# Kernel optimization log

Measured on AMD Instinct MI355X. Metric: run time of the kernel, lower is better.

Reference implementation:

```python
import jax, jax.numpy as jnp
import numpy as np

N = 65536      # num ref nodes
M = 65536      # num query nodes
E = 1572864    # num edges (avg degree 24)
K0 = 27        # num kernels (3x3x3 neighborhood)
D1 = 64        # input channels
D2 = 64        # output channels


def setup_inputs() -> dict:
    key = jax.random.key(0)
    k1, k2, k3, k4, k5, k6 = jax.random.split(key, 6)
    # kernel init mirrors initialize_kernel_weight (uniform in [-bound, bound])
    fan_in = D1 * K0
    gain = float(np.sqrt(2.0 / (1.0 + 5.0)))  # leaky_relu gain with slope sqrt(5)
    std = gain / np.sqrt(fan_in)
    bound = float(np.sqrt(3.0) * std)
    kernel = jax.random.uniform(k1, (K0, D1, D2), minval=-bound, maxval=bound, dtype=jnp.float32)
    ref_feat = jax.random.normal(k2, (N, D1), dtype=jnp.float32)
    e_kernel = jax.random.randint(k3, (E,), 0, K0)
    e_ref = jax.random.randint(k4, (E,), 0, N)
    e_query = jax.random.randint(k5, (E,), 0, M)
    e_weight = jax.random.uniform(k6, (E,), dtype=jnp.float32)
    return {
        "kernel": kernel,
        "ref_feat": ref_feat,
        "e_kernel": e_kernel,
        "e_ref": e_ref,
        "e_query": e_query,
        "num_queries": M,
        "e_weight": e_weight,
    }


def reference(kernel, ref_feat, e_kernel, e_ref, e_query, num_queries, e_weight):
    # Math of MessagePassing.forward:
    #   query_feat[m] = sum_{edges e: e_query[e]==m} w_e * (ref_feat[e_ref[e]] @ kernel[e_kernel[e]])
    # Efficient form: precompute each node's transform under every kernel
    # (N*K0*D1*D2 dense GEMM), then gather per edge and scatter-reduce.
    transformed = jnp.einsum('nd,kdo->nko', ref_feat, kernel)   # [N, K0, D2]
    msgs = transformed[e_ref, e_kernel] * e_weight[:, None]      # [E, D2]
    query_feat = jax.ops.segment_sum(msgs, e_query, num_segments=num_queries)  # [M, D2]
    return query_feat
```

## Files before the change

kernel.cpp:

```cpp
#include <hip/hip_runtime.h>

#define DIN 64
#define DOUT 64
#define MAXK 32
#define KSPLIT 8
#define KS4 5
#define QG 128

typedef __bf16 bf16x8 __attribute__((ext_vector_type(8)));
typedef float  f32x4  __attribute__((ext_vector_type(4)));
typedef unsigned int u32x4 __attribute__((ext_vector_type(4)));

static __device__ inline unsigned short f2b(float x) {
    return __builtin_bit_cast(unsigned short, (__bf16)x);
}
static __device__ inline float b2f(unsigned short u) {
    return __uint_as_float(((unsigned int)u) << 16);
}

__global__ __launch_bounds__(256) void pre_kernel(
    const float* __restrict__ W, unsigned short* __restrict__ Wt, int total,
    const int* __restrict__ eq, int E, int* __restrict__ qcount, int HB)
{
    const int t = threadIdx.x;
    if ((int)blockIdx.x < HB) {
        __shared__ int l[512];
        l[t] = 0; l[t + 256] = 0;
        __syncthreads();
        const int stride = HB * 256;
        for (int i = (int)blockIdx.x * 256 + t; i < E; i += stride)
            atomicAdd(&l[((unsigned)eq[i]) >> 7], 1);
        __syncthreads();
        int v0 = l[t];       if (v0) atomicAdd(&qcount[t], v0);
        int v1 = l[t + 256]; if (v1) atomicAdd(&qcount[t + 256], v1);
    } else {
        int i = ((int)blockIdx.x - HB) * 256 + t;
        if (i < total) {
            int j    = i & 7;
            int lane = (i >> 3) & 63;
            int h    = (i >> 9) & 1;
            int tt   = (i >> 10) & 3;
            int k    = i >> 12;
            int col  = lane & 15;
            int quad = lane >> 4;
            int d1 = h * 32 + quad * 8 + j;
            int d2 = tt * 16 + col;
            Wt[i] = f2b(W[(k * 64 + d1) * 64 + d2]);
        }
    }
}

__global__ void p1_scan_kernel(const int* __restrict__ qcount,
                               int* __restrict__ gbase, int* __restrict__ gcursor,
                               int* __restrict__ qstart, int NB, int M, int E) {
    __shared__ int sh[1024];
    int t = threadIdx.x;
    int v = (t < NB) ? qcount[t] : 0;
    sh[t] = v;
    __syncthreads();
    #pragma unroll
    for (int o = 1; o < 1024; o <<= 1) {
        int x = (t >= o) ? sh[t - o] : 0;
        __syncthreads();
        sh[t] += x;
        __syncthreads();
    }
    int ex = sh[t] - v;
    if (t < NB) { gbase[t] = ex; gcursor[t] = ex; }
    if (t == 0) qstart[M] = E;
}


static __device__ __forceinline__ void phaseA_body16(
    const float* __restrict__ ref,
    const unsigned short* __restrict__ Wt,
    unsigned short* __restrict__ T,
    int K0, int Nn, int nblk, int k0, int k1, char* lds)
{
    const int t    = threadIdx.x;
    const int lane = t & 63;
    const int wid  = t >> 6;
    const int col  = lane & 15;
    const int quad = lane >> 4;
    const int n0   = nblk * 256 + wid * 16;
    const int row  = n0 + col;
    char* buf = lds + wid * 2304;

    const float* rp = ref + (size_t)row * 64;
    f32x4 r0 = *reinterpret_cast<const f32x4*>(rp + quad * 8);
    f32x4 r1 = *reinterpret_cast<const f32x4*>(rp + quad * 8 + 4);
    f32x4 r2 = *reinterpret_cast<const f32x4*>(rp + 32 + quad * 8);
    f32x4 r3 = *reinterpret_cast<const f32x4*>(rp + 32 + quad * 8 + 4);
    bf16x8 b0, b1;
    #pragma unroll
    for (int i = 0; i < 4; ++i) {
        b0[i]     = (__bf16)r0[i];
        b0[4 + i] = (__bf16)r1[i];
        b1[i]     = (__bf16)r2[i];
        b1[4 + i] = (__bf16)r3[i];
    }

    const int rrow = lane >> 2;
    const int rq   = lane & 3;

    for (int k = k0; k < k1; ++k) {
        const unsigned short* Wk = Wt + (size_t)k * 4096;
        #pragma unroll
        for (int tt = 0; tt < 4; ++tt) {
            const unsigned short* ap = Wk + (size_t)tt * 1024 + lane * 8;
            bf16x8 a0 = *reinterpret_cast<const bf16x8*>(ap);
            bf16x8 a1 = *reinterpret_cast<const bf16x8*>(ap + 512);
            f32x4 c = {0.f, 0.f, 0.f, 0.f};
            c = __builtin_amdgcn_mfma_f32_16x16x32_bf16(a0, b0, c, 0, 0, 0);
            c = __builtin_amdgcn_mfma_f32_16x16x32_bf16(a1, b1, c, 0, 0, 0);
            unsigned int lo = (unsigned int)f2b(c[0]) | ((unsigned int)f2b(c[1]) << 16);
            unsigned int hi = (unsigned int)f2b(c[2]) | ((unsigned int)f2b(c[3]) << 16);
            *reinterpret_cast<uint2*>(buf + col * 144 + tt * 32 + quad * 8) =
                make_uint2(lo, hi);
        }
        u32x4 v0 = *reinterpret_cast<const u32x4*>(buf + rrow * 144 + rq * 32);
        u32x4 v1 = *reinterpret_cast<const u32x4*>(buf + rrow * 144 + rq * 32 + 16);
        size_t gb = ((size_t)k * Nn + n0 + rrow) * 64 + rq * 16;
        *reinterpret_cast<u32x4*>(T + gb)     = v0;
        *reinterpret_cast<u32x4*>(T + gb + 8) = v1;
    }
}


__global__ __launch_bounds__(1024) void fusedA_scatter_kernel(
    const float* __restrict__ ref, const unsigned short* __restrict__ Wt,
    unsigned short* __restrict__ T, int K0, int Nn, int SCB, int NA2,
    const int* __restrict__ eq, const int* __restrict__ er,
    const int* __restrict__ ek, const float* __restrict__ ew,
    int E, int* __restrict__ gcursor, uint2* __restrict__ tmp)
{
    __shared__ __align__(16) char ldsbuf[16 * 2304];
    __shared__ int bin[512];
    __shared__ int base[512];
    const int t = threadIdx.x;

    if ((int)blockIdx.x < SCB) {
        if (t < 512) bin[t] = 0;
        __syncthreads();
        const int i0 = (int)blockIdx.x * 8192;
        unsigned key[8];
        unsigned rank[8];
        uint2 pay[8];
        #pragma unroll
        for (int u = 0; u < 8; ++u) {
            int i = i0 + u * 1024 + t;
            if (i < E) {
                int q = eq[i];
                unsigned b = ((unsigned)q) >> 7;
                key[u] = b;
                rank[u] = atomicAdd(&bin[b], 1);
                pay[u] = make_uint2((unsigned)er[i] | ((unsigned)ek[i] << 16) |
                                    ((unsigned)(q & (QG - 1)) << 21),
                                    __float_as_uint(ew[i]));
            } else {
                key[u] = 0xFFFFFFFFu;
            }
        }
        __syncthreads();
        if (t < 512) {
            int c = bin[t];
            if (c) base[t] = atomicAdd(&gcursor[t], c);
        }
        __syncthreads();
        #pragma unroll
        for (int u = 0; u < 8; ++u) {
            if (key[u] != 0xFFFFFFFFu)
                tmp[(size_t)base[key[u]] + rank[u]] = pay[u];
        }
    } else {
        const int ab   = (int)blockIdx.x - SCB;
        const int nblk = ab % NA2;
        const int ky   = ab / NA2;
        const int kch  = (K0 + KSPLIT - 1) / KSPLIT;
        const int k0   = ky * kch;
        if (k0 >= K0) return;
        int k1 = k0 + kch;
        if (k1 > K0) k1 = K0;
        phaseA_body16(ref, Wt, T, K0, Nn, nblk, k0, k1, ldsbuf);
    }
}

__global__ __launch_bounds__(1024) void fusedA_p2_kernel(
    const float* __restrict__ ref, const unsigned short* __restrict__ Wt,
    unsigned short* __restrict__ T, int K0, int Nn, int NB, int NA2,
    const uint2* __restrict__ tmp, const int* __restrict__ gbase,
    const int* __restrict__ qcount, uint2* __restrict__ rec,
    int* __restrict__ qstart)
{
    __shared__ __align__(16) char ldsbuf[16 * 2304];
    __shared__ int fine[QG];
    __shared__ int foff[QG];
    __shared__ int vsave[QG];
    const int t = threadIdx.x;

    if ((int)blockIdx.x < NB) {
        const int b = (int)blockIdx.x;
        const int s = gbase[b];
        const int L = qcount[b];
        if (t < QG) fine[t] = 0;
        __syncthreads();
        for (int i = t; i < L; i += 1024)
            atomicAdd(&fine[(tmp[s + i].x >> 21) & (QG - 1)], 1);
        __syncthreads();
        if (t < QG) vsave[t] = fine[t];
        __syncthreads();
        #pragma unroll
        for (int o = 1; o < QG; o <<= 1) {
            int x = (t >= o && t < QG) ? fine[t - o] : 0;
            __syncthreads();
            if (t < QG) fine[t] += x;
            __syncthreads();
        }
        if (t < QG) {
            int ex = fine[t] - vsave[t];
            foff[t] = ex;
            qstart[b * QG + t] = s + ex;
            fine[t] = 0;
        }
        __syncthreads();
        for (int i = t; i < L; i += 1024) {
            uint2 p = tmp[s + i];
            unsigned fb = (p.x >> 21) & (QG - 1);
            int r = atomicAdd(&fine[fb], 1);
            rec[(size_t)s + foff[fb] + r] = p;
        }
    } else {
        const int ab   = (int)blockIdx.x - NB;
        const int nblk = ab % NA2;
        const int ky   = KS4 + ab / NA2;
        const int kch  = (K0 + KSPLIT - 1) / KSPLIT;
        const int k0   = ky * kch;
        if (k0 >= K0) return;
        int k1 = k0 + kch;
        if (k1 > K0) k1 = K0;
        phaseA_body16(ref, Wt, T, K0, Nn, nblk, k0, k1, ldsbuf);
    }
}


__global__ __launch_bounds__(256) void phaseB_kernel(
    const unsigned short* __restrict__ T,
    const uint2* __restrict__ rec,
    const int* __restrict__ qstart,
    float* __restrict__ out, int Nn)
{
    const int lane = threadIdx.x & 63;
    const int wid  = threadIdx.x >> 6;
    const int q    = blockIdx.x * 4 + wid;

    int beg = qstart[q];
    int end = qstart[q + 1];
    int cnt = end - beg;
    float acc = 0.f;

    if (cnt <= 64) {
        uint2 rv = make_uint2(0u, 0u);
        if (lane < cnt) rv = rec[beg + lane];
        int j = 0;
        for (; j + 8 <= cnt; j += 8) {
            float partial[8];
            #pragma unroll
            for (int u = 0; u < 8; ++u) {
                unsigned mx = (unsigned)__builtin_amdgcn_readlane((int)rv.x, j + u);
                unsigned mw = (unsigned)__builtin_amdgcn_readlane((int)rv.y, j + u);
                unsigned off = (((mx >> 16) & 31) * (unsigned)Nn + (mx & 0xFFFFu)) * 64u
                               + (unsigned)lane;
                partial[u] = __uint_as_float(mw) * b2f(T[off]);
            }
            #pragma unroll
            for (int u = 0; u < 8; ++u) acc += partial[u];
        }
        for (; j < cnt; ++j) {
            unsigned mx = (unsigned)__builtin_amdgcn_readlane((int)rv.x, j);
            unsigned mw = (unsigned)__builtin_amdgcn_readlane((int)rv.y, j);
            unsigned off = (((mx >> 16) & 31) * (unsigned)Nn + (mx & 0xFFFFu)) * 64u
                           + (unsigned)lane;
            acc = fmaf(__uint_as_float(mw), b2f(T[off]), acc);
        }
    } else {
        for (int j = beg; j < end; ++j) {
            uint2 v0 = rec[j];
            unsigned m0 = __builtin_amdgcn_readfirstlane(v0.x);
            float w0 = __uint_as_float(__builtin_amdgcn_readfirstlane(v0.y));
            unsigned off = (((m0 >> 16) & 31) * (unsigned)Nn + (m0 & 0xFFFFu)) * 64u
                           + (unsigned)lane;
            acc = fmaf(w0, b2f(T[off]), acc);
        }
    }
    out[(size_t)q * 64 + lane] = acc;
}


__global__ void hist_kernel(const int* __restrict__ ek, int E, int* __restrict__ counts) {
    __shared__ int l[MAXK];
    if (threadIdx.x < MAXK) l[threadIdx.x] = 0;
    __syncthreads();
    int stride = gridDim.x * blockDim.x;
    for (int i = blockIdx.x * blockDim.x + threadIdx.x; i < E; i += stride)
        atomicAdd(&l[ek[i]], 1);
    __syncthreads();
    if (threadIdx.x < MAXK) {
        int v = l[threadIdx.x];
        if (v) atomicAdd(&counts[threadIdx.x], v);
    }
}

__global__ void scan_kernel(const int* __restrict__ counts, int K,
                            int* __restrict__ start, int* __restrict__ cursor) {
    if (threadIdx.x == 0 && blockIdx.x == 0) {
        int acc = 0;
        for (int k = 0; k < K; ++k) {
            start[k] = acc;
            cursor[k] = acc;
            acc += counts[k];
        }
    }
}

__global__ void scatter_kernel(const int* __restrict__ ek, int E,
                               int* __restrict__ cursor, int* __restrict__ sorted) {
    __shared__ int lcnt[MAXK], lbase[MAXK], lpos[MAXK];
    if (threadIdx.x < MAXK) { lcnt[threadIdx.x] = 0; lpos[threadIdx.x] = 0; }
    __syncthreads();
    int i = blockIdx.x * blockDim.x + threadIdx.x;
    int k = 0;
    bool valid = (i < E);
    if (valid) { k = ek[i]; atomicAdd(&lcnt[k], 1); }
    __syncthreads();
    if (threadIdx.x < MAXK) {
        int v = lcnt[threadIdx.x];
        if (v) lbase[threadIdx.x] = atomicAdd(&cursor[threadIdx.x], v);
    }
    __syncthreads();
    if (valid) {
        int slot = lbase[k] + atomicAdd(&lpos[k], 1);
        sorted[slot] = i;
    }
}

__global__ __launch_bounds__(256) void mp_bucket_kernel(
    const float* __restrict__ W, const float* __restrict__ ref,
    const int* __restrict__ e_ref, const int* __restrict__ e_query,
    const float* __restrict__ e_weight, const int* __restrict__ sorted,
    const int* __restrict__ start, const int* __restrict__ counts,
    float* __restrict__ out)
{
    const int k = blockIdx.y;
    const int lane = threadIdx.x & 63;
    const int wid = threadIdx.x >> 6;

    float wreg[DIN];
    const float* Wk = W + k * DIN * DOUT;
    #pragma unroll
    for (int d = 0; d < DIN; ++d) wreg[d] = Wk[d * DOUT + lane];

    const int s = start[k];
    const int c = counts[k];
    const int nwaves = gridDim.x * 4;

    for (int i = blockIdx.x * 4 + wid; i < c; i += nwaves) {
        int eid = __builtin_amdgcn_readfirstlane(sorted[s + i]);
        int r = e_ref[eid];
        int q = e_query[eid];
        float w = e_weight[eid];
        const float* row = ref + r * DIN;
        float a0 = 0.f, a1 = 0.f, a2 = 0.f, a3 = 0.f;
        #pragma unroll
        for (int d = 0; d < DIN; d += 4) {
            a0 += row[d + 0] * wreg[d + 0];
            a1 += row[d + 1] * wreg[d + 1];
            a2 += row[d + 2] * wreg[d + 2];
            a3 += row[d + 3] * wreg[d + 3];
        }
        atomicAdd(&out[q * DOUT + lane], ((a0 + a1) + (a2 + a3)) * w);
    }
}


extern "C" void kernel_launch(void* const* d_in, const int* in_sizes, int n_in,
                              void* d_out, int out_size, void* d_ws, size_t ws_size,
                              hipStream_t stream) {
    const float* W        = (const float*)d_in[0];
    const float* ref      = (const float*)d_in[1];
    const int*   e_kernel = (const int*)d_in[2];
    const int*   e_ref    = (const int*)d_in[3];
    const int*   e_query  = (const int*)d_in[4];
    const float* e_weight = (const float*)d_in[6];

    const int K0 = in_sizes[0] / (DIN * DOUT);
    const int N  = in_sizes[1] / DIN;
    const int E  = in_sizes[2];
    const int M  = out_size / DOUT;
    const int KD = K0 * 64;
    const int NB = M / QG;

    float* out = (float*)d_out;

    size_t off = 0;
    auto alloc = [&](size_t bytes, size_t align) {
        off = (off + align - 1) / align * align;
        size_t r = off; off += bytes; return r;
    };
    size_t o_tmp     = alloc((size_t)E * 8, 16);
    size_t o_rec     = alloc((size_t)E * 8, 16);
    size_t o_qstart  = alloc((size_t)(M + 1) * 4, 4);
    size_t o_qcount  = alloc(1024 * 4, 4);
    size_t o_gbase   = alloc(1024 * 4, 4);
    size_t o_gcursor = alloc(1024 * 4, 4);
    size_t o_wt      = alloc((size_t)K0 * 4096 * 2, 16);
    size_t o_T       = alloc((size_t)N * KD * 2, 16);
    size_t needA = off;

    bool planA_ok = (ws_size >= needA) && (M % QG == 0) && (NB >= 1) && (NB <= 512) &&
                    (N % 256 == 0) && (N <= 65536) && (K0 <= 32);

    if (planA_ok) {
        char* ws = (char*)d_ws;
        uint2* tmp           = (uint2*)(ws + o_tmp);
        uint2* rec           = (uint2*)(ws + o_rec);
        int*  qstart         = (int*)(ws + o_qstart);
        int*  qcount         = (int*)(ws + o_qcount);
        int*  gbase          = (int*)(ws + o_gbase);
        int*  gcursor        = (int*)(ws + o_gcursor);
        unsigned short* Wt   = (unsigned short*)(ws + o_wt);
        unsigned short* T    = (unsigned short*)(ws + o_T);

        const int HB   = 512;
        const int CWB  = (K0 * 4096 + 255) / 256;
        const int SCB  = (E + 8191) / 8192;
        const int NA2  = N / 256;

        hipMemsetAsync(qcount, 0, 1024 * sizeof(int), stream);

        pre_kernel<<<HB + CWB, 256, 0, stream>>>(W, Wt, K0 * 4096,
                                                 e_query, E, qcount, HB);

        p1_scan_kernel<<<1, 1024, 0, stream>>>(qcount, gbase, gcursor, qstart, NB, M, E);

        fusedA_scatter_kernel<<<SCB + NA2 * KS4, 1024, 0, stream>>>(
            ref, Wt, T, K0, N, SCB, NA2,
            e_query, e_ref, e_kernel, e_weight, E, gcursor, tmp);

        fusedA_p2_kernel<<<NB + NA2 * (KSPLIT - KS4), 1024, 0, stream>>>(
            ref, Wt, T, K0, N, NB, NA2,
            tmp, gbase, qcount, rec, qstart);

        phaseB_kernel<<<M / 4, 256, 0, stream>>>(T, rec, qstart, out, N);
    } else {
        hipMemsetAsync(out, 0, (size_t)out_size * sizeof(float), stream);
        size_t needB = (size_t)(96 + E) * sizeof(int);
        if (ws_size >= needB) {
            int* ws_i   = (int*)d_ws;
            int* counts = ws_i;
            int* start  = ws_i + 32;
            int* cursor = ws_i + 64;
            int* sorted = ws_i + 96;
            hipMemsetAsync(counts, 0, 96 * sizeof(int), stream);
            hist_kernel<<<512, 256, 0, stream>>>(e_kernel, E, counts);
            scan_kernel<<<1, 64, 0, stream>>>(counts, K0, start, cursor);
            scatter_kernel<<<(E + 255) / 256, 256, 0, stream>>>(e_kernel, E, cursor, sorted);
            dim3 grid(64, K0);
            mp_bucket_kernel<<<grid, 256, 0, stream>>>(W, ref, e_ref, e_query, e_weight,
                                                       sorted, start, counts, out);
        }
    }
}
```

Before: 274.9 us.

## Fold scan into scatter kernel and skip unused transformed rows via usage map

Removes the separate single-block scan launch: each scatter block redoes the 512-entry prefix scan of the bucket counts itself and adds it to a zero-based cursor. The scatter pass also marks which (kernel, ref node) pairs are touched by any edge in a byte map, and the second-phase GEMM blocks skip the T stores for untouched rows. The k-range split between the two fused kernels changes from 8 slices to fixed 4-kernel chunks with the first 12 kernels in the first launch. This adds a memset of the map and a redundant scan per scatter block. With random edges about 41% of rows are untouched, so only part of the T writes in the second kernel are saved.

```diff
diff --git a/kernel.cpp b/kernel.cpp
--- a/kernel.cpp
+++ b/kernel.cpp
@@ -3,9 +3,8 @@
 #define DIN 64
 #define DOUT 64
 #define MAXK 32
-#define KSPLIT 8
-#define KS4 5
 #define QG 128
+#define KCH 4
 
 typedef __bf16 bf16x8 __attribute__((ext_vector_type(8)));
 typedef float  f32x4  __attribute__((ext_vector_type(4)));
@@ -17,6 +16,7 @@
 static __device__ inline float b2f(unsigned short u) {
     return __uint_as_float(((unsigned int)u) << 16);
 }
+
 
 __global__ __launch_bounds__(256) void pre_kernel(
     const float* __restrict__ W, unsigned short* __restrict__ Wt, int total,
@@ -50,32 +50,14 @@
     }
 }
 
-__global__ void p1_scan_kernel(const int* __restrict__ qcount,
-                               int* __restrict__ gbase, int* __restrict__ gcursor,
-                               int* __restrict__ qstart, int NB, int M, int E) {
-    __shared__ int sh[1024];
-    int t = threadIdx.x;
-    int v = (t < NB) ? qcount[t] : 0;
-    sh[t] = v;
-    __syncthreads();
-    #pragma unroll
-    for (int o = 1; o < 1024; o <<= 1) {
-        int x = (t >= o) ? sh[t - o] : 0;
-        __syncthreads();
-        sh[t] += x;
-        __syncthreads();
-    }
-    int ex = sh[t] - v;
-    if (t < NB) { gbase[t] = ex; gcursor[t] = ex; }
-    if (t == 0) qstart[M] = E;
-}
-
-
+
+template <bool MAPPED>
 static __device__ __forceinline__ void phaseA_body16(
     const float* __restrict__ ref,
     const unsigned short* __restrict__ Wt,
+    const unsigned char* __restrict__ map,
     unsigned short* __restrict__ T,
-    int K0, int Nn, int nblk, int k0, int k1, char* lds)
+    int Nn, int nblk, int k0, int k1, char* lds)
 {
     const int t    = threadIdx.x;
     const int lane = t & 63;
@@ -104,6 +86,8 @@
     const int rq   = lane & 3;
 
     for (int k = k0; k < k1; ++k) {
+        unsigned char use = 1;
+        if (MAPPED) use = map[(size_t)k * Nn + n0 + rrow];
         const unsigned short* Wk = Wt + (size_t)k * 4096;
         #pragma unroll
         for (int tt = 0; tt < 4; ++tt) {
@@ -120,28 +104,47 @@
         }
         u32x4 v0 = *reinterpret_cast<const u32x4*>(buf + rrow * 144 + rq * 32);
         u32x4 v1 = *reinterpret_cast<const u32x4*>(buf + rrow * 144 + rq * 32 + 16);
-        size_t gb = ((size_t)k * Nn + n0 + rrow) * 64 + rq * 16;
-        *reinterpret_cast<u32x4*>(T + gb)     = v0;
-        *reinterpret_cast<u32x4*>(T + gb + 8) = v1;
-    }
-}
-
-
-__global__ __launch_bounds__(1024) void fusedA_scatter_kernel(
+        if (use) {
+            size_t gb = ((size_t)k * Nn + n0 + rrow) * 64 + rq * 16;
+            *reinterpret_cast<u32x4*>(T + gb)     = v0;
+            *reinterpret_cast<u32x4*>(T + gb + 8) = v1;
+        }
+    }
+}
+
+
+__global__ __launch_bounds__(1024) void fused_scat_kernel(
     const float* __restrict__ ref, const unsigned short* __restrict__ Wt,
-    unsigned short* __restrict__ T, int K0, int Nn, int SCB, int NA2,
+    unsigned short* __restrict__ T, int K0, int Nn, int SCB, int NA2, int K1,
     const int* __restrict__ eq, const int* __restrict__ er,
     const int* __restrict__ ek, const float* __restrict__ ew,
-    int E, int* __restrict__ gcursor, uint2* __restrict__ tmp)
+    int E, const int* __restrict__ qcount, int* __restrict__ gbase,
+    int* __restrict__ gcursor, int* __restrict__ qstart, int M,
+    uint2* __restrict__ tmp, unsigned char* __restrict__ map)
 {
     __shared__ __align__(16) char ldsbuf[16 * 2304];
+    __shared__ int sh[512];
     __shared__ int bin[512];
     __shared__ int base[512];
     const int t = threadIdx.x;
 
     if ((int)blockIdx.x < SCB) {
+        int v = 0;
+        if (t < 512) { v = qcount[t]; sh[t] = v; }
+        __syncthreads();
+        #pragma unroll
+        for (int o = 1; o < 512; o <<= 1) {
+            int x = (t >= o && t < 512) ? sh[t - o] : 0;
+            __syncthreads();
+            if (t < 512) sh[t] += x;
+            __syncthreads();
+        }
+        if (t < 512) sh[t] -= v;
+        if ((int)blockIdx.x == 0 && t < 512) gbase[t] = sh[t];
+        if ((int)blockIdx.x == 0 && t == 0) qstart[M] = E;
         if (t < 512) bin[t] = 0;
         __syncthreads();
+
         const int i0 = (int)blockIdx.x * 8192;
         unsigned key[8];
         unsigned rank[8];
@@ -150,13 +153,16 @@
         for (int u = 0; u < 8; ++u) {
             int i = i0 + u * 1024 + t;
             if (i < E) {
-                int q = eq[i];
+                int q  = eq[i];
+                int rr = er[i];
+                int kk = ek[i];
                 unsigned b = ((unsigned)q) >> 7;
                 key[u] = b;
                 rank[u] = atomicAdd(&bin[b], 1);
-                pay[u] = make_uint2((unsigned)er[i] | ((unsigned)ek[i] << 16) |
+                pay[u] = make_uint2((unsigned)rr | ((unsigned)kk << 16) |
                                     ((unsigned)(q & (QG - 1)) << 21),
                                     __float_as_uint(ew[i]));
+                map[(size_t)kk * Nn + rr] = 1;
             } else {
                 key[u] = 0xFFFFFFFFu;
             }
@@ -164,7 +170,7 @@
         __syncthreads();
         if (t < 512) {
             int c = bin[t];
-            if (c) base[t] = atomicAdd(&gcursor[t], c);
+            if (c) base[t] = sh[t] + atomicAdd(&gcursor[t], c);
         }
         __syncthreads();
         #pragma unroll
@@ -175,19 +181,20 @@
     } else {
         const int ab   = (int)blockIdx.x - SCB;
         const int nblk = ab % NA2;
-        const int ky   = ab / NA2;
-        const int kch  = (K0 + KSPLIT - 1) / KSPLIT;
-        const int k0   = ky * kch;
-        if (k0 >= K0) return;
-        int k1 = k0 + kch;
-        if (k1 > K0) k1 = K0;
-        phaseA_body16(ref, Wt, T, K0, Nn, nblk, k0, k1, ldsbuf);
-    }
-}
-
-__global__ __launch_bounds__(1024) void fusedA_p2_kernel(
+        const int sl   = ab / NA2;
+        const int k0   = sl * KCH;
+        if (k0 >= K1) return;
+        int k1 = k0 + KCH;
+        if (k1 > K1) k1 = K1;
+        phaseA_body16<false>(ref, Wt, nullptr, T, Nn, nblk, k0, k1, ldsbuf);
+    }
+}
+
+
+__global__ __launch_bounds__(1024) void fused_p2_kernel(
     const float* __restrict__ ref, const unsigned short* __restrict__ Wt,
-    unsigned short* __restrict__ T, int K0, int Nn, int NB, int NA2,
+    const unsigned char* __restrict__ map, unsigned short* __restrict__ T,
+    int K0, int Nn, int NB, int NA2, int K1,
     const uint2* __restrict__ tmp, const int* __restrict__ gbase,
     const int* __restrict__ qcount, uint2* __restrict__ rec,
     int* __restrict__ qstart)
@@ -232,13 +239,12 @@
     } else {
         const int ab   = (int)blockIdx.x - NB;
         const int nblk = ab % NA2;
-        const int ky   = KS4 + ab / NA2;
-        const int kch  = (K0 + KSPLIT - 1) / KSPLIT;
-        const int k0   = ky * kch;
+        const int sl   = ab / NA2;
+        const int k0   = K1 + sl * KCH;
         if (k0 >= K0) return;
-        int k1 = k0 + kch;
+        int k1 = k0 + KCH;
         if (k1 > K0) k1 = K0;
-        phaseA_body16(ref, Wt, T, K0, Nn, nblk, k0, k1, ldsbuf);
+        phaseA_body16<true>(ref, Wt, map, T, Nn, nblk, k0, k1, ldsbuf);
     }
 }
 
@@ -409,9 +415,11 @@
     size_t o_tmp     = alloc((size_t)E * 8, 16);
     size_t o_rec     = alloc((size_t)E * 8, 16);
     size_t o_qstart  = alloc((size_t)(M + 1) * 4, 4);
-    size_t o_qcount  = alloc(1024 * 4, 4);
-    size_t o_gbase   = alloc(1024 * 4, 4);
-    size_t o_gcursor = alloc(1024 * 4, 4);
+    size_t o_gbase   = alloc(512 * 4, 4);
+    size_t o_qcount  = alloc(512 * 4, 4);
+    size_t o_gcursor = alloc(512 * 4, 4);
+    size_t o_map     = alloc((size_t)K0 * N, 4);
+    size_t zero_end  = off;
     size_t o_wt      = alloc((size_t)K0 * 4096 * 2, 16);
     size_t o_T       = alloc((size_t)N * KD * 2, 16);
     size_t needA = off;
@@ -424,9 +432,10 @@
         uint2* tmp           = (uint2*)(ws + o_tmp);
         uint2* rec           = (uint2*)(ws + o_rec);
         int*  qstart         = (int*)(ws + o_qstart);
+        int*  gbase          = (int*)(ws + o_gbase);
         int*  qcount         = (int*)(ws + o_qcount);
-        int*  gbase          = (int*)(ws + o_gbase);
         int*  gcursor        = (int*)(ws + o_gcursor);
+        unsigned char* map   = (unsigned char*)(ws + o_map);
         unsigned short* Wt   = (unsigned short*)(ws + o_wt);
         unsigned short* T    = (unsigned short*)(ws + o_T);
 
@@ -434,20 +443,22 @@
         const int CWB  = (K0 * 4096 + 255) / 256;
         const int SCB  = (E + 8191) / 8192;
         const int NA2  = N / 256;
-
-        hipMemsetAsync(qcount, 0, 1024 * sizeof(int), stream);
+        const int K1   = (K0 < 12) ? K0 : 12;
+        const int NS1  = (K1 + KCH - 1) / KCH;
+        const int NS2  = (K0 - K1 + KCH - 1) / KCH;
+
+        hipMemsetAsync(ws + o_qcount, 0, zero_end - o_qcount, stream);
 
         pre_kernel<<<HB + CWB, 256, 0, stream>>>(W, Wt, K0 * 4096,
                                                  e_query, E, qcount, HB);
 
-        p1_scan_kernel<<<1, 1024, 0, stream>>>(qcount, gbase, gcursor, qstart, NB, M, E);
-
-        fusedA_scatter_kernel<<<SCB + NA2 * KS4, 1024, 0, stream>>>(
-            ref, Wt, T, K0, N, SCB, NA2,
-            e_query, e_ref, e_kernel, e_weight, E, gcursor, tmp);
-
-        fusedA_p2_kernel<<<NB + NA2 * (KSPLIT - KS4), 1024, 0, stream>>>(
-            ref, Wt, T, K0, N, NB, NA2,
+        fused_scat_kernel<<<SCB + NA2 * NS1, 1024, 0, stream>>>(
+            ref, Wt, T, K0, N, SCB, NA2, K1,
+            e_query, e_ref, e_kernel, e_weight, E,
+            qcount, gbase, gcursor, qstart, M, tmp, map);
+
+        fused_p2_kernel<<<NB + NA2 * NS2, 1024, 0, stream>>>(
+            ref, Wt, map, T, K0, N, NB, NA2, K1,
             tmp, gbase, qcount, rec, qstart);
 
         phaseB_kernel<<<M / 4, 256, 0, stream>>>(T, rec, qstart, out, N);
```

New measurement: 299.2 us. 8.8% more time.
